# Kernel tuning notes

Measured on AMD Instinct MI355X. Metric: run time of the kernel, lower is better.

## Reference

```python
import jax, jax.numpy as jnp
import numpy as np

IMAGE_W = IMAGE_H = 608
TOP_N = 1000
MIN_SCORE = 0.05
NMS_THR = 0.5
MAX_DET = 100
B = 8
NUM_CLASSES = 80
STRIDES = [32, 16, 8]
ANCHOR_WH = {32: [[116, 90], [156, 198], [373, 326]],
             16: [[30, 61], [62, 45], [59, 119]],
             8: [[10, 13], [16, 30], [33, 23]]}


def _make_anchors(stride):
    # anchors layout [B,g,g,3,5] = (grid_x, grid_y, anchor_w*stride, anchor_h*stride, stride)
    g = IMAGE_W // stride
    ys, xs = jnp.meshgrid(jnp.arange(g, dtype=jnp.float32),
                          jnp.arange(g, dtype=jnp.float32), indexing='ij')
    grid = jnp.broadcast_to(jnp.stack([xs, ys], -1)[:, :, None, :], (g, g, 3, 2))
    wh = jnp.asarray(ANCHOR_WH[stride], dtype=jnp.float32) * stride
    wh = jnp.broadcast_to(wh[None, None, :, :], (g, g, 3, 2))
    s = jnp.full((g, g, 3, 1), float(stride), dtype=jnp.float32)
    a = jnp.concatenate([grid, wh, s], -1)
    return jnp.broadcast_to(a[None], (B, g, g, 3, 5))


def setup_inputs() -> dict:
    key = jax.random.key(0)
    ks = jax.random.split(key, 9)
    inp = {}
    for i, stride in enumerate(STRIDES):
        g = IMAGE_W // stride
        inp[f'obj{i}'] = jax.random.normal(ks[3 * i + 0], (B, g, g, 3, 1), jnp.float32)
        inp[f'reg{i}'] = jax.random.normal(ks[3 * i + 1], (B, g, g, 3, 4), jnp.float32)
        inp[f'cls{i}'] = jax.random.normal(ks[3 * i + 2], (B, g, g, 3, NUM_CLASSES), jnp.float32)
        inp[f'anchors{i}'] = _make_anchors(stride)
    return inp


def _decode_level(obj, reg, cls, anch):
    Bn = obj.shape[0]
    obj = jax.nn.sigmoid(obj.reshape(Bn, -1))                       # [B,N]
    cls = jax.nn.sigmoid(cls.reshape(Bn, -1, cls.shape[-1]))        # [B,N,C]
    reg = reg.reshape(Bn, -1, 4)
    anch = anch.reshape(Bn, -1, 5)
    ctr = (jax.nn.sigmoid(reg[..., 0:2]) + anch[..., 0:2]) * anch[..., 4:5]
    wh = jnp.exp(reg[..., 2:4]) * anch[..., 2:4] / anch[..., 4:5]
    x1y1 = ctr - 0.5 * wh
    x2y2 = wh + x1y1
    boxes = jnp.concatenate([x1y1, x2y2], -1).astype(jnp.int32)     # trunc toward zero == torch .int()
    boxes = jnp.stack([jnp.maximum(boxes[..., 0], 0),
                       jnp.maximum(boxes[..., 1], 0),
                       jnp.minimum(boxes[..., 2], IMAGE_W - 1),
                       jnp.minimum(boxes[..., 3], IMAGE_H - 1)], -1)
    scores = jnp.max(cls, axis=-1) * obj
    classes = jnp.argmax(cls, axis=-1).astype(jnp.int32)
    if scores.shape[1] >= TOP_N:
        scores, idx = jax.lax.top_k(scores, TOP_N)
        classes = jnp.take_along_axis(classes, idx, axis=1)
        boxes = jnp.take_along_axis(boxes, idx[..., None], axis=1)
    return scores, classes, boxes


def _nms_one_image(scores, classes, boxes):
    # scores [N], classes int32 [N], boxes int32 [N,4]
    N = scores.shape[0]
    valid = scores > MIN_SCORE
    s = jnp.where(valid, scores, -1.0)
    order = jnp.argsort(-s)
    s = s[order]
    valid = valid[order]
    cls_f = classes[order].astype(jnp.float32)
    b = boxes[order].astype(jnp.float32)
    areas = (b[:, 2] - b[:, 0]) * (b[:, 3] - b[:, 1])
    idxs = jnp.arange(N)

    def body(i, keep):
        box = b[i]
        xx1 = jnp.maximum(box[0], b[:, 0])
        yy1 = jnp.maximum(box[1], b[:, 1])
        xx2 = jnp.minimum(box[2], b[:, 2])
        yy2 = jnp.minimum(box[3], b[:, 3])
        inter = jnp.maximum(xx2 - xx1, 0.0) * jnp.maximum(yy2 - yy1, 0.0)
        iou = inter / (areas[i] + areas - inter)
        suppress = keep[i] & (idxs > i) & (iou > NMS_THR)
        return keep & ~suppress

    keep = jax.lax.fori_loop(0, N, body, valid)
    pos = jnp.cumsum(keep) - 1                       # output slot of each kept box
    slot = jnp.where(keep & (pos < MAX_DET), pos, MAX_DET)  # overflow/dropped -> dump slot
    out_s = jnp.full((MAX_DET + 1,), -1.0, jnp.float32).at[slot].set(s)[:MAX_DET]
    out_c = jnp.full((MAX_DET + 1,), -1.0, jnp.float32).at[slot].set(cls_f)[:MAX_DET]
    out_b = jnp.full((MAX_DET + 1, 4), -1.0, jnp.float32).at[slot].set(b)[:MAX_DET]
    return out_s, out_c, out_b


def _forward(obj0, obj1, obj2, reg0, reg1, reg2, cls0, cls1, cls2,
             anchors0, anchors1, anchors2):
    objs = [obj0, obj1, obj2]
    regs = [reg0, reg1, reg2]
    clss = [cls0, cls1, cls2]
    anchs = [anchors0, anchors1, anchors2]
    sc, cl, bx = [], [], []
    for o, r, c, a in zip(objs, regs, clss, anchs):
        s_, c_, b_ = _decode_level(o, r, c, a)
        sc.append(s_); cl.append(c_); bx.append(b_)
    scores = jnp.concatenate(sc, axis=1)
    classes = jnp.concatenate(cl, axis=1)
    boxes = jnp.concatenate(bx, axis=1)
    return jax.vmap(_nms_one_image)(scores, classes, boxes)


def reference(obj0, obj1, obj2, reg0, reg1, reg2, cls0, cls1, cls2,
              anchors0, anchors1, anchors2):
    return _forward(obj0, obj1, obj2, reg0, reg1, reg2, cls0, cls1, cls2,
                    anchors0, anchors1, anchors2)
```

## Files before the change

kernel.cpp:

```cpp
#include <hip/hip_runtime.h>
#include <math.h>

constexpr int BATCH   = 8;
constexpr int NUM_CLS = 80;
constexpr int N0 = 19 * 19 * 3;
constexpr int N1 = 38 * 38 * 3;
constexpr int N2 = 76 * 76 * 3;
constexpr int OFF1 = N0;
constexpr int OFF2 = N0 + N1;
constexpr int NTOT = N0 + N1 + N2;
constexpr int TOPN = 1000;
constexpr int NSEL = 3 * TOPN;
constexpr int MAXDET = 100;
constexpr float MIN_SCORE_F = 0.05f;
constexpr int IMG_MAX = 607;

__device__ __forceinline__ float sigmoidf_(float x) {
    return 1.0f / (1.0f + expf(-x));
}

__constant__ float AWH[3][3][2] = {
    {{116.f, 90.f}, {156.f, 198.f}, {373.f, 326.f}},
    {{ 30.f, 61.f}, { 62.f,  45.f}, { 59.f, 119.f}},
    {{ 10.f, 13.f}, { 16.f,  30.f}, { 33.f,  23.f}},
};

__device__ __forceinline__ bool iou_gt(float4 a, float4 c) {
    float ai = (a.z - a.x) * (a.w - a.y);
    float aj = (c.z - c.x) * (c.w - c.y);
    float xx1 = fmaxf(a.x, c.x);
    float yy1 = fmaxf(a.y, c.y);
    float xx2 = fminf(a.z, c.z);
    float yy2 = fminf(a.w, c.w);
    float inter = fmaxf(xx2 - xx1, 0.0f) * fmaxf(yy2 - yy1, 0.0f);
    float uni = ai + aj - inter;
    return (inter > 0.5f * uni) && (inter > 0.0f);
}

__global__ __launch_bounds__(256) void k_decode(
    const float* __restrict__ obj0, const float* __restrict__ reg0,
    const float* __restrict__ cls0,
    const float* __restrict__ obj1, const float* __restrict__ reg1,
    const float* __restrict__ cls1,
    const float* __restrict__ obj2, const float* __restrict__ reg2,
    const float* __restrict__ cls2,
    unsigned long long* __restrict__ decKey, float* __restrict__ decC,
    float* __restrict__ decB, int* __restrict__ gflagImg, int* __restrict__ fbCursor,
    int* __restrict__ lvlDone)
{
    if (blockIdx.x == 0 && threadIdx.x < 32) {
        if (threadIdx.x < 8)  gflagImg[threadIdx.x] = 0;
        if (threadIdx.x < 8)  lvlDone[threadIdx.x] = 0;
        if (threadIdx.x < 24) fbCursor[threadIdx.x] = 0;
    }

    __shared__ float sBest[64];
    __shared__ int   sCls[64];

    int g0 = blockIdx.x * 64;
    int t  = threadIdx.x;

    {
        int q  = t >> 2;
        int lq = t & 3;
        int idx = g0 + q;
        if (idx < BATCH * NTOT) {
            int b  = idx / NTOT;
            int na = idx - b * NTOT;
            const float* cls; int Nl, n;
            if (na < OFF1)      { cls = cls0; Nl = N0; n = na; }
            else if (na < OFF2) { cls = cls1; Nl = N1; n = na - OFF1; }
            else                { cls = cls2; Nl = N2; n = na - OFF2; }
            size_t bn = (size_t)b * Nl + n;

            const float4* cv = reinterpret_cast<const float4*>(cls + bn * NUM_CLS);
            float best = -1.0f; int bc = 0;
            #pragma unroll
            for (int k = 0; k < 5; ++k) {
                int m = lq + 4 * k;
                float4 v = cv[m];
                float s;
                s = sigmoidf_(v.x); if (s > best) { best = s; bc = 4 * m + 0; }
                s = sigmoidf_(v.y); if (s > best) { best = s; bc = 4 * m + 1; }
                s = sigmoidf_(v.z); if (s > best) { best = s; bc = 4 * m + 2; }
                s = sigmoidf_(v.w); if (s > best) { best = s; bc = 4 * m + 3; }
            }
            #pragma unroll
            for (int d = 1; d <= 2; d <<= 1) {
                float ob = __shfl_xor(best, d);
                int   oc = __shfl_xor(bc, d);
                if (ob > best || (ob == best && oc < bc)) { best = ob; bc = oc; }
            }
            if (lq == 0) { sBest[q] = best; sCls[q] = bc; }
        }
    }
    __syncthreads();

    if (t < 64) {
        int idx = g0 + t;
        if (idx < BATCH * NTOT) {
            int b  = idx / NTOT;
            int na = idx - b * NTOT;
            const float *obj, *reg;
            int Nl, n, lvl, g;
            float st;
            if (na < OFF1)      { obj = obj0; reg = reg0; Nl = N0; n = na;        lvl = 0; g = 19; st = 32.f; }
            else if (na < OFF2) { obj = obj1; reg = reg1; Nl = N1; n = na - OFF1; lvl = 1; g = 38; st = 16.f; }
            else                { obj = obj2; reg = reg2; Nl = N2; n = na - OFF2; lvl = 2; g = 76; st = 8.f;  }
            size_t bn = (size_t)b * Nl + n;

            float so    = sigmoidf_(obj[bn]);
            float score = sBest[t] * so;
            int   bc    = sCls[t];

            int a    = n % 3;
            int cell = n / 3;
            int gx   = cell % g;
            int gy   = cell / g;
            float ax = (float)gx, ay = (float)gy;
            float aw = AWH[lvl][a][0], ah = AWH[lvl][a][1];

            float4 rv = reinterpret_cast<const float4*>(reg)[bn];
            float cx = (sigmoidf_(rv.x) + ax) * st;
            float cy = (sigmoidf_(rv.y) + ay) * st;
            float w  = expf(rv.z) * aw;
            float h  = expf(rv.w) * ah;
            float x1f = cx - 0.5f * w;
            float y1f = cy - 0.5f * h;
            float x2f = w + x1f;
            float y2f = h + y1f;
            int x1 = (int)x1f, y1 = (int)y1f, x2 = (int)x2f, y2 = (int)y2f;
            x1 = (x1 < 0) ? 0 : x1;
            y1 = (y1 < 0) ? 0 : y1;
            x2 = (x2 > IMG_MAX) ? IMG_MAX : x2;
            y2 = (y2 > IMG_MAX) ? IMG_MAX : y2;

            size_t gg = (size_t)b * NTOT + na;
            decKey[gg] = ((unsigned long long)__float_as_uint(score) << 15) | (unsigned)(Nl - n);
            decC[gg] = (float)bc;
            reinterpret_cast<float4*>(decB)[gg] =
                make_float4((float)x1, (float)y1, (float)x2, (float)y2);
        }
    }
}

constexpr int NBIN  = 4096;
constexpr int STCAP = 2048;

__global__ __launch_bounds__(1024) void k_select_nms(
    const unsigned long long* __restrict__ decKey, const float* __restrict__ decC,
    const float* __restrict__ decB, float* __restrict__ selS, float* __restrict__ selC,
    float* __restrict__ selB, unsigned long long* __restrict__ selKey,
    int* __restrict__ gflagImg, int* __restrict__ fbCursor,
    int* __restrict__ lvlDone, float* __restrict__ out)
{
    __shared__ union LdsU {
        struct {
            unsigned hist[NBIN];
            unsigned cum[NBIN];
            unsigned wscan[32];
            unsigned long long stKey[STCAP];
            int stIdx[STCAP];
        } sel;
        struct {
            union { unsigned long long keys[NSEL]; float4 boxes[NSEL]; } U;
            int ord[NSEL];
        } nms;
    } L;
    __shared__ float4 keptBox[MAXDET];
    __shared__ int keptRank[MAXDET];
    __shared__ int sTot; __shared__ int sOvf;
    __shared__ int sBstar; __shared__ int sNeed;
    __shared__ int sPos; __shared__ int sNValid;

    int b   = blockIdx.x / 3;
    int lvl = blockIdx.x % 3;
    int off = (lvl == 0) ? 0 : (lvl == 1) ? OFF1 : OFF2;
    int Nl  = (lvl == 0) ? N0 : (lvl == 1) ? N1 : N2;
    int tid = threadIdx.x;
    int lane = tid & 63;
    int wv   = tid >> 6;

    {
        unsigned* hist = L.sel.hist;
        unsigned* cum  = L.sel.cum;
        unsigned* wscan = L.sel.wscan;
        unsigned long long* stKey = L.sel.stKey;
        int* stIdx = L.sel.stIdx;

        const unsigned long long* keys = decKey + (size_t)b * NTOT + off;

        for (int t = tid; t < NBIN; t += 1024) hist[t] = 0;
        if (tid == 0) { sTot = 0; sOvf = 0; }
        __syncthreads();

        for (int t = tid; t < Nl; t += 1024)
            atomicAdd(&hist[(unsigned)(keys[t] >> 33)], 1u);
        __syncthreads();

        {
            uint4 hh = reinterpret_cast<uint4*>(hist)[tid];
            reinterpret_cast<uint4*>(hist)[tid] = make_uint4(0u, 0u, 0u, 0u);
            unsigned ssum = hh.x + hh.y + hh.z + hh.w;

            unsigned sfx = ssum;
            #pragma unroll
            for (int d = 1; d < 64; d <<= 1) {
                unsigned o = __shfl_down(sfx, d);
                if (lane + d < 64) sfx += o;
            }
            if (lane == 0) wscan[wv] = sfx;
            __syncthreads();
            if (tid < 16) {
                unsigned v = wscan[tid];
                unsigned s2 = v;
                #pragma unroll
                for (int d = 1; d < 16; d <<= 1) {
                    unsigned o = __shfl_down(s2, d);
                    if (tid + d < 16) s2 += o;
                }
                wscan[16 + tid] = s2 - v;
            }
            __syncthreads();
            unsigned Tt = wscan[16 + wv] + (sfx - ssum);
            unsigned c3 = Tt;
            unsigned c2 = c3 + hh.w;
            unsigned c1 = c2 + hh.z;
            unsigned c0 = c1 + hh.y;
            reinterpret_cast<uint4*>(cum)[tid] = make_uint4(c0, c1, c2, c3);
        }
        __syncthreads();

        for (int t = tid; t < Nl; t += 1024) {
            unsigned long long k = keys[t];
            unsigned bin = (unsigned)(k >> 33);
            if (cum[bin] < (unsigned)TOPN) {
                unsigned c = atomicAdd(&hist[bin], 1u);
                unsigned p = cum[bin] + c;
                if (p < STCAP) { stKey[p] = k; stIdx[p] = t; }
                else sOvf = 1;
            }
        }
        __syncthreads();

        {
            uint4 hh = reinterpret_cast<uint4*>(hist)[tid];
            uint4 cc = reinterpret_cast<uint4*>(cum)[tid];
            unsigned loc = 0;
            if (cc.x < (unsigned)TOPN) loc += hh.x;
            if (cc.y < (unsigned)TOPN) loc += hh.y;
            if (cc.z < (unsigned)TOPN) loc += hh.z;
            if (cc.w < (unsigned)TOPN) loc += hh.w;
            #pragma unroll
            for (int d = 1; d < 64; d <<= 1) loc += __shfl_down(loc, d);
            if (lane == 0 && loc) atomicAdd(&sTot, (int)loc);
        }
        __syncthreads();

        auto writeOut = [&](int t, int r) {
            size_t g = (size_t)b * NTOT + off + t;
            unsigned long long k = keys[t];
            float sraw = __uint_as_float((unsigned)(k >> 15));
            float strn = (sraw > MIN_SCORE_F) ? sraw : -1.0f;
            int G = off + t;
            unsigned long long gk =
                ((unsigned long long)(__float_as_uint(sraw) | 0x80000000u) << 16) |
                (unsigned)(NTOT - G);
            int o = b * NSEL + lvl * TOPN + r;
            selS[o] = strn;
            selC[o] = decC[g];
            selKey[o] = gk;
            reinterpret_cast<float4*>(selB)[o] = reinterpret_cast<const float4*>(decB)[g];
        };

        if (sOvf == 0) {
            int M = sTot;
            for (int p = tid; p < M; p += 1024) {
                unsigned long long k = stKey[p];
                unsigned bin = (unsigned)(k >> 33);
                unsigned start = cum[bin], end = start + hist[bin];
                int r = (int)start;
                for (unsigned q = start; q < end; ++q) r += (stKey[q] > k) ? 1 : 0;
                if (r < TOPN) writeOut(stIdx[p], r);
            }
        } else {
            if (tid == 0) {
                gflagImg[b] = 1;
                int B = 0;
                for (int bin = NBIN - 1; bin >= 0; --bin) {
                    if (cum[bin] <= (unsigned)(TOPN - 1) &&
                        cum[bin] + hist[bin] > (unsigned)(TOPN - 1)) { B = bin; break; }
                }
                sBstar = B; sNeed = TOPN - (int)cum[B];
            }
            __syncthreads();
            int Bstar = sBstar, need = sNeed;
            for (int t = tid; t < Nl; t += 1024) {
                unsigned long long k = keys[t];
                int bin = (int)(unsigned)(k >> 33);
                bool em = false;
                if (bin > Bstar) em = true;
                else if (bin == Bstar) {
                    int r = 0;
                    for (int j = 0; j < Nl; ++j) {
                        unsigned long long kj = keys[j];
                        r += ((int)(unsigned)(kj >> 33) == Bstar && kj > k) ? 1 : 0;
                    }
                    em = (r < need);
                }
                if (em) {
                    int r = atomicAdd(&fbCursor[b * 3 + lvl], 1);
                    writeOut(t, r);
                }
            }
        }
    }

    __threadfence();
    __syncthreads();
    if (tid == 0) atomicAdd(&lvlDone[b], 1);

    if (lvl != 0) return;

    if (tid == 0) {
        while (atomicAdd(&lvlDone[b], 0) < 3) __builtin_amdgcn_s_sleep(8);
    }
    __syncthreads();
    __threadfence();

    auto& U = L.nms.U;
    int* ord = L.nms.ord;
    const float* S = selS + b * NSEL;

    for (int t = tid; t < NSEL; t += 1024) U.keys[t] = selKey[b * NSEL + t];
    if (tid == 0) sNValid = 0;
    __syncthreads();
    int fb = gflagImg[b];

    int myT[3], myR[3];
    int nMine = 0;
    int nvLoc = 0;
    for (int t = tid; t < NSEL; t += 1024) {
        unsigned long long k = U.keys[t];
        int rank;
        if (!fb) {
            int l = t / TOPN;
            rank = t - l * TOPN;
            #pragma unroll
            for (int m = 0; m < 3; ++m) {
                if (m == l) continue;
                int base = m * TOPN, lo = 0, hi = TOPN;
                while (lo < hi) {
                    int mid = (lo + hi) >> 1;
                    if (U.keys[base + mid] > k) lo = mid + 1; else hi = mid;
                }
                rank += lo;
            }
        } else {
            int r = 0;
            for (int j = 0; j < NSEL; ++j) r += (U.keys[j] > k) ? 1 : 0;
            rank = r;
        }
        myT[nMine] = t; myR[nMine] = rank; nMine++;
        if (S[t] > MIN_SCORE_F) nvLoc++;
    }
    #pragma unroll
    for (int d = 1; d < 64; d <<= 1) nvLoc += __shfl_down(nvLoc, d);
    if ((tid & 63) == 0 && nvLoc) atomicAdd(&sNValid, nvLoc);
    __syncthreads();

    for (int q = 0; q < nMine; ++q) {
        float4 bb = reinterpret_cast<const float4*>(selB)[b * NSEL + myT[q]];
        U.boxes[myR[q]] = bb;
        ord[myR[q]] = myT[q];
    }
    __syncthreads();

    if (tid < 64) {
        int nValid = sNValid;
        int pos = 0;
        int nW = (nValid + 63) >> 6;
        for (int w = 0; w < nW && pos < MAXDET; ++w) {
            int j = w * 64 + lane;
            float4 bx = (j < NSEL) ? U.boxes[j]
                                   : make_float4(4e8f, 4e8f, -4e8f, -4e8f);
            bool valid = (j < nValid);
            bool sup = false;
            for (int q = 0; q < pos; ++q)
                sup = sup || iou_gt(keptBox[q], bx);
            unsigned long long live = __ballot(valid && !sup);
            while (live) {
                int p = __ffsll(live) - 1;
                if (lane == 0) keptRank[pos] = w * 64 + p;
                if (lane == p) keptBox[pos] = bx;
                pos++;
                if (pos >= MAXDET) break;
                float kx = __shfl(bx.x, p), ky = __shfl(bx.y, p);
                float kz = __shfl(bx.z, p), kw = __shfl(bx.w, p);
                bool hit = iou_gt(make_float4(kx, ky, kz, kw), bx);
                live &= ~__ballot(hit);
                live &= ~(1ull << p);
            }
        }
        if (lane == 0) sPos = pos;
    }
    __syncthreads();

    int pos = sPos;
    const float* C = selC + b * NSEL;
    float* out_s = out + b * MAXDET;
    float* out_c = out + BATCH * MAXDET + b * MAXDET;
    float* out_b = out + 2 * BATCH * MAXDET + (size_t)b * MAXDET * 4;
    for (int t = tid; t < MAXDET; t += 1024) {
        if (t < pos) {
            int i = keptRank[t];
            int o = ord[i];
            float4 bb = U.boxes[i];
            out_s[t] = S[o];
            out_c[t] = C[o];
            out_b[t * 4 + 0] = bb.x; out_b[t * 4 + 1] = bb.y;
            out_b[t * 4 + 2] = bb.z; out_b[t * 4 + 3] = bb.w;
        } else {
            out_s[t] = -1.0f; out_c[t] = -1.0f;
            out_b[t * 4 + 0] = -1.0f; out_b[t * 4 + 1] = -1.0f;
            out_b[t * 4 + 2] = -1.0f; out_b[t * 4 + 3] = -1.0f;
        }
    }
}

extern "C" void kernel_launch(void* const* d_in, const int* in_sizes, int n_in,
                              void* d_out, int out_size, void* d_ws, size_t ws_size,
                              hipStream_t stream) {
    (void)n_in; (void)out_size; (void)ws_size;

    bool dict = (in_sizes[2] == BATCH * N0 * NUM_CLS);
    const float *obj[3], *reg[3], *cls[3];
    for (int l = 0; l < 3; ++l) {
        obj[l] = (const float*)d_in[dict ? 4 * l + 0 : l];
        reg[l] = (const float*)d_in[dict ? 4 * l + 1 : 3 + l];
        cls[l] = (const float*)d_in[dict ? 4 * l + 2 : 6 + l];
    }

    char* ws = (char*)d_ws;
    size_t off = 0;
    auto take = [&](size_t bytes) -> void* {
        void* p = ws + off;
        off += (bytes + 255) & ~(size_t)255;
        return p;
    };
    int*                 gflagImg = (int*)take(BATCH * sizeof(int));
    int*                 fbCursor = (int*)take(BATCH * 3 * sizeof(int));
    int*                 lvlDone  = (int*)take(BATCH * sizeof(int));
    unsigned long long*  decKey   = (unsigned long long*)take((size_t)BATCH * NTOT * 8);
    float*               decC     = (float*)take((size_t)BATCH * NTOT * 4);
    float*               decB     = (float*)take((size_t)BATCH * NTOT * 16);
    float*               selS     = (float*)take((size_t)BATCH * NSEL * 4);
    float*               selC     = (float*)take((size_t)BATCH * NSEL * 4);
    float*               selB     = (float*)take((size_t)BATCH * NSEL * 16);
    unsigned long long*  selKey   = (unsigned long long*)take((size_t)BATCH * NSEL * 8);

    int totalDec = BATCH * NTOT;
    k_decode<<<(totalDec + 63) / 64, 256, 0, stream>>>(
        obj[0], reg[0], cls[0],
        obj[1], reg[1], cls[1],
        obj[2], reg[2], cls[2],
        decKey, decC, decB, gflagImg, fbCursor, lvlDone);

    k_select_nms<<<BATCH * 3, 1024, 0, stream>>>(decKey, decC, decB,
                                                 selS, selC, selB, selKey,
                                                 gflagImg, fbCursor, lvlDone,
                                                 (float*)d_out);
}
```

Measured before the change: 182.1 us.

## Fuse per-level selection into one block per image, dropping cross-block spin sync

The select/NMS kernel now launches one 1024-thread block per image instead of one per image-level. Each block loops over the three levels in turn, with the fallback flag and cursor kept in shared memory. This removes the global atomics, the thread fences and the spin-wait on the level-0 block, along with their workspace resets in the decode kernel. The cost is that the three level selections no longer run in parallel, which leaves fewer active CUs and puts the level work in series within each block.

```diff
diff --git a/kernel.cpp b/kernel.cpp
--- a/kernel.cpp
+++ b/kernel.cpp
@@ -45,15 +45,8 @@
     const float* __restrict__ obj2, const float* __restrict__ reg2,
     const float* __restrict__ cls2,
     unsigned long long* __restrict__ decKey, float* __restrict__ decC,
-    float* __restrict__ decB, int* __restrict__ gflagImg, int* __restrict__ fbCursor,
-    int* __restrict__ lvlDone)
+    float* __restrict__ decB)
 {
-    if (blockIdx.x == 0 && threadIdx.x < 32) {
-        if (threadIdx.x < 8)  gflagImg[threadIdx.x] = 0;
-        if (threadIdx.x < 8)  lvlDone[threadIdx.x] = 0;
-        if (threadIdx.x < 24) fbCursor[threadIdx.x] = 0;
-    }
-
     __shared__ float sBest[64];
     __shared__ int   sCls[64];
 
@@ -147,12 +140,11 @@
 constexpr int NBIN  = 4096;
 constexpr int STCAP = 2048;
 
-__global__ __launch_bounds__(1024) void k_select_nms(
+__global__ __launch_bounds__(1024) void k_fused(
     const unsigned long long* __restrict__ decKey, const float* __restrict__ decC,
     const float* __restrict__ decB, float* __restrict__ selS, float* __restrict__ selC,
     float* __restrict__ selB, unsigned long long* __restrict__ selKey,
-    int* __restrict__ gflagImg, int* __restrict__ fbCursor,
-    int* __restrict__ lvlDone, float* __restrict__ out)
+    float* __restrict__ out)
 {
     __shared__ union LdsU {
         struct {
@@ -172,16 +164,20 @@
     __shared__ int sTot; __shared__ int sOvf;
     __shared__ int sBstar; __shared__ int sNeed;
     __shared__ int sPos; __shared__ int sNValid;
-
-    int b   = blockIdx.x / 3;
-    int lvl = blockIdx.x % 3;
-    int off = (lvl == 0) ? 0 : (lvl == 1) ? OFF1 : OFF2;
-    int Nl  = (lvl == 0) ? N0 : (lvl == 1) ? N1 : N2;
+    __shared__ int sFbImg;
+    __shared__ int sFbCur;
+
+    int b   = blockIdx.x;
     int tid = threadIdx.x;
     int lane = tid & 63;
     int wv   = tid >> 6;
 
-    {
+    if (tid == 0) sFbImg = 0;
+
+    for (int lvl = 0; lvl < 3; ++lvl) {
+        int off = (lvl == 0) ? 0 : (lvl == 1) ? OFF1 : OFF2;
+        int Nl  = (lvl == 0) ? N0 : (lvl == 1) ? N1 : N2;
+
         unsigned* hist = L.sel.hist;
         unsigned* cum  = L.sel.cum;
         unsigned* wscan = L.sel.wscan;
@@ -190,8 +186,9 @@
 
         const unsigned long long* keys = decKey + (size_t)b * NTOT + off;
 
+        __syncthreads();
         for (int t = tid; t < NBIN; t += 1024) hist[t] = 0;
-        if (tid == 0) { sTot = 0; sOvf = 0; }
+        if (tid == 0) { sTot = 0; sOvf = 0; sFbCur = 0; }
         __syncthreads();
 
         for (int t = tid; t < Nl; t += 1024)
@@ -285,7 +282,7 @@
             }
         } else {
             if (tid == 0) {
-                gflagImg[b] = 1;
+                sFbImg = 1;
                 int B = 0;
                 for (int bin = NBIN - 1; bin >= 0; --bin) {
                     if (cum[bin] <= (unsigned)(TOPN - 1) &&
@@ -309,24 +306,13 @@
                     em = (r < need);
                 }
                 if (em) {
-                    int r = atomicAdd(&fbCursor[b * 3 + lvl], 1);
+                    int r = atomicAdd(&sFbCur, 1);
                     writeOut(t, r);
                 }
             }
         }
     }
-
-    __threadfence();
-    __syncthreads();
-    if (tid == 0) atomicAdd(&lvlDone[b], 1);
-
-    if (lvl != 0) return;
-
-    if (tid == 0) {
-        while (atomicAdd(&lvlDone[b], 0) < 3) __builtin_amdgcn_s_sleep(8);
-    }
-    __syncthreads();
-    __threadfence();
+    __syncthreads();
 
     auto& U = L.nms.U;
     int* ord = L.nms.ord;
@@ -335,7 +321,7 @@
     for (int t = tid; t < NSEL; t += 1024) U.keys[t] = selKey[b * NSEL + t];
     if (tid == 0) sNValid = 0;
     __syncthreads();
-    int fb = gflagImg[b];
+    int fb = sFbImg;
 
     int myT[3], myR[3];
     int nMine = 0;
@@ -448,9 +434,6 @@
         off += (bytes + 255) & ~(size_t)255;
         return p;
     };
-    int*                 gflagImg = (int*)take(BATCH * sizeof(int));
-    int*                 fbCursor = (int*)take(BATCH * 3 * sizeof(int));
-    int*                 lvlDone  = (int*)take(BATCH * sizeof(int));
     unsigned long long*  decKey   = (unsigned long long*)take((size_t)BATCH * NTOT * 8);
     float*               decC     = (float*)take((size_t)BATCH * NTOT * 4);
     float*               decB     = (float*)take((size_t)BATCH * NTOT * 16);
@@ -464,10 +447,9 @@
         obj[0], reg[0], cls[0],
         obj[1], reg[1], cls[1],
         obj[2], reg[2], cls[2],
-        decKey, decC, decB, gflagImg, fbCursor, lvlDone);
-
-    k_select_nms<<<BATCH * 3, 1024, 0, stream>>>(decKey, decC, decB,
-                                                 selS, selC, selB, selKey,
-                                                 gflagImg, fbCursor, lvlDone,
-                                                 (float*)d_out);
+        decKey, decC, decB);
+
+    k_fused<<<BATCH, 1024, 0, stream>>>(decKey, decC, decB,
+                                        selS, selC, selB, selKey,
+                                        (float*)d_out);
 }
```

Result: slower. 195.7 us (+7.4%).
